# Kernel optimization log

Hardware: AMD Instinct MI355X
Metric: run time of the kernel (lower is better)

## Reference

```python
import jax, jax.numpy as jnp
import numpy as np

DIM = 512
DIM_HEAD = 32
HEADS = DIM // DIM_HEAD
WS = 8  # window (partition) size
INNER = (DIM * 4 * 2 // 3 // 32) * 32  # gated-MLP inner dim = 2720
EPS = 1e-6
LS_INIT = 1e-5


def _ln(x, g, b):
    mu = jnp.mean(x, axis=-1, keepdims=True)
    var = jnp.var(x, axis=-1, keepdims=True)
    return (x - mu) * jax.lax.rsqrt(var + EPS) * g + b


def setup_inputs() -> dict:
    key = jax.random.key(0)
    ks = jax.random.split(key, 8)
    B, H, W = 8, 96, 96
    s = lambda d: 1.0 / np.sqrt(d)
    return {
        "x": jax.random.normal(ks[0], (B, H, W, DIM), jnp.float32),
        "norm1_g": jnp.ones((DIM,), jnp.float32),
        "norm1_b": jnp.zeros((DIM,), jnp.float32),
        "qkv_w": jax.random.normal(ks[1], (DIM, 3 * DIM), jnp.float32) * s(DIM),
        "qkv_b": jnp.zeros((3 * DIM,), jnp.float32),
        "proj_w": jax.random.normal(ks[2], (DIM, DIM), jnp.float32) * s(DIM),
        "proj_b": jnp.zeros((DIM,), jnp.float32),
        "ls1": jnp.full((DIM,), LS_INIT, jnp.float32),
        "norm2_g": jnp.ones((DIM,), jnp.float32),
        "norm2_b": jnp.zeros((DIM,), jnp.float32),
        "glu_w": jax.random.normal(ks[3], (DIM, 2 * INNER), jnp.float32) * s(DIM),
        "glu_b": jnp.zeros((2 * INNER,), jnp.float32),
        "fc2_w": jax.random.normal(ks[4], (INNER, DIM), jnp.float32) * s(INNER),
        "fc2_b": jnp.zeros((DIM,), jnp.float32),
        "ls2": jnp.full((DIM,), LS_INIT, jnp.float32),
    }


def reference(x, norm1_g, norm1_b, qkv_w, qkv_b, proj_w, proj_b, ls1,
              norm2_g, norm2_b, glu_w, glu_b, fc2_w, fc2_b, ls2):
    B, H, W, C = x.shape
    nH, nW = H // WS, W // WS
    T = WS * WS  # tokens per window

    # ---- window attention branch ----
    y = _ln(x, norm1_g, norm1_b)
    # window_partition: (B,H,W,C) -> (B*nH*nW, T, C)
    y = y.reshape(B, nH, WS, nW, WS, C).transpose(0, 1, 3, 2, 4, 5)
    y = y.reshape(-1, T, C)
    qkv = y @ qkv_w + qkv_b                      # (M, T, 3C)
    qkv = qkv.reshape(-1, T, 3, HEADS, DIM_HEAD)
    q, k, v = qkv[:, :, 0], qkv[:, :, 1], qkv[:, :, 2]   # (M, T, h, d)
    scale = DIM_HEAD ** -0.5
    attn = jnp.einsum('mqhd,mkhd->mhqk', q, k) * scale
    attn = jax.nn.softmax(attn, axis=-1)
    o = jnp.einsum('mhqk,mkhd->mqhd', attn, v).reshape(-1, T, C)
    o = o @ proj_w + proj_b
    # window_reverse: (M, T, C) -> (B, H, W, C)
    o = o.reshape(B, nH, nW, WS, WS, C).transpose(0, 1, 3, 2, 4, 5)
    o = o.reshape(B, H, W, C)
    x = x + ls1 * o

    # ---- gated MLP branch (GLU with SiLU) ----
    y = _ln(x, norm2_g, norm2_b)
    h = y @ glu_w + glu_b
    h, gate = jnp.split(h, 2, axis=-1)
    h = h * jax.nn.silu(gate)
    h = h @ fc2_w + fc2_b
    x = x + ls2 * h
    return x
```

## Files before the change

### kernel.cpp

```cpp
#include <hip/hip_runtime.h>
#include <hip/hip_bf16.h>
#include <stdint.h>
#include <math.h>

#define DIM 512
#define INNER 1344
#define INNERP 1408

typedef __attribute__((ext_vector_type(8))) short vbf8;
typedef __attribute__((ext_vector_type(4))) float vf4;
typedef __attribute__((ext_vector_type(4))) int v4i;
typedef __attribute__((ext_vector_type(8))) int v8i;

typedef __attribute__((address_space(1))) void as1void;
typedef __attribute__((address_space(3))) void as3void;

union frag8 {
  v8i w;
  v4i h[2];
};

__device__ __forceinline__ uint32_t quant4(float v) {
  uint32_t s = (__float_as_uint(v) >> 31) << 3;
  float a = fabsf(v);
  uint32_t m = (a > 0.25f) + (a > 0.75f) + (a > 1.25f) + (a > 1.75f) +
               (a > 2.5f) + (a > 3.5f) + (a > 5.0f);
  return s | m;
}
__device__ __forceinline__ uint32_t pack8fp4(const float* r) {
  uint32_t u = 0;
#pragma unroll
  for (int j = 0; j < 8; ++j) u |= quant4(r[j]) << (4 * j);
  return u;
}

#define MFMA4(a, b, c, sb) \
  __builtin_amdgcn_mfma_scale_f32_16x16x128_f8f6f4((a), (b), (c), 4, 4, 0, 127, 0, (sb))

__global__ void k_transpose4(const float* __restrict__ Wsrc, uint8_t* __restrict__ WT,
                             uint8_t* __restrict__ Wsc, int K, int N, int ldB, int ldS,
                             int nsplit) {
  __shared__ float tile[32][33];
  const int tx = threadIdx.x, ty = threadIdx.y;
  const int n0 = blockIdx.x * 32, k0 = blockIdx.y * 32;
#pragma unroll
  for (int i = 0; i < 32; i += 8) {
    int k = k0 + ty + i, n = n0 + tx;
    if (k < K && n < N) tile[ty + i][tx] = Wsrc[(size_t)k * N + n];
  }
  __syncthreads();
  if (tx < 16) {
#pragma unroll
    for (int i = 0; i < 32; i += 8) {
      int n = n0 + ty + i;
      if (n >= N) continue;
      float v0 = tile[2 * tx][ty + i], v1 = tile[2 * tx + 1][ty + i];
      float m = fmaxf(fabsf(v0), fabsf(v1));
      m = fmaxf(m, __shfl_xor(m, 1));
      m = fmaxf(m, __shfl_xor(m, 2));
      m = fmaxf(m, __shfl_xor(m, 4));
      m = fmaxf(m, __shfl_xor(m, 8));
      uint8_t sbyte;
      float s;
      if (m < 1e-20f) {
        sbyte = 0;
        s = 0.0f;
      } else {
        int e = (int)ceilf(log2f(m * 0.166666672f));
        e = e < -126 ? -126 : (e > 126 ? 126 : e);
        sbyte = (uint8_t)(e + 127);
        s = exp2f((float)(-e));
      }
      int np = n + (n >= nsplit ? 64 : 0);
      WT[(size_t)np * ldB + (k0 >> 1) + tx] =
          (uint8_t)(quant4(v0 * s) | (quant4(v1 * s) << 4));
      if (tx == 0) Wsc[(size_t)np * ldS + (k0 >> 5)] = sbyte;
    }
  }
}

__global__ void k_padbias(const float* __restrict__ b, float* __restrict__ o) {
  int c = blockIdx.x * 256 + threadIdx.x;
  if (c < INNER) o[c] = b[c];
  else if (c >= INNERP && c < INNERP + INNER) o[c] = b[c - 64];
  else if (c < 2816) o[c] = 0.0f;
}

template <bool PART, bool BF16IN>
__global__ __launch_bounds__(256) void k_ln(const void* __restrict__ xin,
                                            const float* __restrict__ gw,
                                            const float* __restrict__ bw,
                                            uint8_t* __restrict__ y) {
  const int wave = threadIdx.x >> 6, lane = threadIdx.x & 63;
  const int tok = blockIdx.x * 4 + wave;
  float vals[8];
  if (BF16IN) {
    const __hip_bfloat16* xr = (const __hip_bfloat16*)xin + (size_t)tok * DIM + lane * 8;
    union {
      vbf8 v;
      ushort e[8];
    } u;
    u.v = *(const vbf8*)xr;
#pragma unroll
    for (int j = 0; j < 8; ++j) vals[j] = __uint_as_float((unsigned)u.e[j] << 16);
  } else {
    const float* xr = (const float*)xin + (size_t)tok * DIM + lane * 8;
    const float4 v0 = *(const float4*)xr;
    const float4 v1 = *(const float4*)(xr + 4);
    vals[0] = v0.x; vals[1] = v0.y; vals[2] = v0.z; vals[3] = v0.w;
    vals[4] = v1.x; vals[5] = v1.y; vals[6] = v1.z; vals[7] = v1.w;
  }
  float s = 0.f, ss = 0.f;
#pragma unroll
  for (int j = 0; j < 8; ++j) {
    s += vals[j];
    ss += vals[j] * vals[j];
  }
#pragma unroll
  for (int off = 32; off > 0; off >>= 1) {
    s += __shfl_xor(s, off);
    ss += __shfl_xor(ss, off);
  }
  const float mu = s * (1.0f / DIM);
  const float rs = rsqrtf(ss * (1.0f / DIM) - mu * mu + 1e-6f);
  size_t orow;
  if (PART) {
    int b = tok / 9216, rem = tok % 9216;
    int h = rem / 96, w = rem % 96;
    orow = (size_t)(((b * 12 + (h >> 3)) * 12 + (w >> 3)) * 64 + (h & 7) * 8 + (w & 7));
  } else {
    orow = (size_t)tok;
  }
  const float4 g0 = *(const float4*)(gw + lane * 8);
  const float4 g1 = *(const float4*)(gw + lane * 8 + 4);
  const float4 b0 = *(const float4*)(bw + lane * 8);
  const float4 b1 = *(const float4*)(bw + lane * 8 + 4);
  const float gg[8] = {g0.x, g0.y, g0.z, g0.w, g1.x, g1.y, g1.z, g1.w};
  const float bb[8] = {b0.x, b0.y, b0.z, b0.w, b1.x, b1.y, b1.z, b1.w};
  float r[8];
#pragma unroll
  for (int j = 0; j < 8; ++j) r[j] = (vals[j] - mu) * rs * gg[j] + bb[j];
  *(uint32_t*)(y + orow * 256 + lane * 4) = pack8fp4(r);
}

template <int ROWS>
__device__ __forceinline__ void stage4(const uint8_t* __restrict__ gsrc, int RB, char* lds,
                                       int wave, int lane) {
  constexpr int RPW = ROWS / 4;
  const int r0 = wave * RPW;
  const int srw = lane >> 2, sbk = lane & 3;
  const uint8_t* src = gsrc + (size_t)(r0 + srw) * RB + ((sbk ^ (srw & 3)) << 4);
  char* dst = lds + r0 * 64;
#pragma unroll
  for (int c = 0; c < RPW; c += 16)
    __builtin_amdgcn_global_load_lds((const as1void*)(src + (size_t)c * RB),
                                     (as3void*)(dst + c * 64), 16, 0, 0);
}

template <int MODE, int NT>
__global__ __launch_bounds__(256, 3) void k_gemm4(const uint8_t* __restrict__ A4,
                                                  const uint8_t* __restrict__ B4,
                                                  const uint8_t* __restrict__ Bsc,
                                                  const float* __restrict__ bias,
                                                  void* __restrict__ outp,
                                                  const void* __restrict__ resid,
                                                  const float* __restrict__ lsv, const int K,
                                                  const int ldOut) {
  __shared__ alignas(16) char As[128 * 64];
  __shared__ alignas(16) char Bs[128 * 64];
  const int nwg = gridDim.x;
  int bid = blockIdx.x;
  bid = (bid & 7) * (nwg >> 3) + (bid >> 3);
  const int bm = bid / NT, bn = bid % NT;
  const int tid = threadIdx.x, wave = tid >> 6, lane = tid & 63;
  const int wr = wave >> 1, wc = wave & 1;
  const int cl = lane & 15, g = lane >> 4;
  const int RB = K >> 1, KB = K >> 5, nkt = K >> 7;

  const uint8_t* Ab = A4 + (size_t)bm * 128 * RB;
  const uint8_t* Bb = B4 + (size_t)bn * 128 * RB;

  int aoff[4], boff[4];
  const uint8_t* bscp[4];
#pragma unroll
  for (int i = 0; i < 4; ++i) {
    int ra = wr * 64 + cl + i * 16;
    int rb = wc * 64 + cl + i * 16;
    aoff[i] = ra * 64 + ((g ^ (ra & 3)) << 4);
    boff[i] = rb * 64 + ((g ^ (rb & 3)) << 4);
    bscp[i] = Bsc + (size_t)(bn * 128 + rb) * KB + g;
  }

  frag8 afr[4], bfr[4];
#pragma unroll
  for (int i = 0; i < 4; ++i) {
    afr[i].w = (v8i){0, 0, 0, 0, 0, 0, 0, 0};
    bfr[i].w = (v8i){0, 0, 0, 0, 0, 0, 0, 0};
  }
  vf4 acc[4][4] = {};

  for (int t = 0; t < nkt; ++t) {
    __syncthreads();
    stage4<128>(Ab + t * 64, RB, As, wave, lane);
    stage4<128>(Bb + t * 64, RB, Bs, wave, lane);
    __syncthreads();
    int sb[4];
#pragma unroll
    for (int i = 0; i < 4; ++i) sb[i] = (int)bscp[i][t * 4];
#pragma unroll
    for (int i = 0; i < 4; ++i) {
      afr[i].h[0] = *(const v4i*)(As + aoff[i]);
      bfr[i].h[0] = *(const v4i*)(Bs + boff[i]);
    }
#pragma unroll
    for (int mi = 0; mi < 4; ++mi)
#pragma unroll
      for (int ni = 0; ni < 4; ++ni)
        acc[mi][ni] = MFMA4(afr[mi].w, bfr[ni].w, acc[mi][ni], sb[ni]);
  }

  const int rl = g << 2;
  const int rbase = bm * 128 + wr * 64;
  const int cbase = bn * 128 + wc * 64;
#pragma unroll
  for (int mi = 0; mi < 4; ++mi) {
#pragma unroll
    for (int j = 0; j < 4; ++j) {
      const int r = rbase + mi * 16 + rl + j;
      size_t orow;
      if (MODE == 1) {
        int m = r >> 6, t = r & 63;
        int b = m / 144, mm = m % 144;
        int wh = mm / 12, ww = mm % 12;
        int h = wh * 8 + (t >> 3), w = ww * 8 + (t & 7);
        orow = (size_t)((b * 96 + h) * 96 + w);
      } else {
        orow = (size_t)r;
      }
#pragma unroll
      for (int ni = 0; ni < 4; ++ni) {
        const int c = cbase + ni * 16 + cl;
        const float v = acc[mi][ni][j] + bias[c];
        if (MODE == 0) {
          ((__hip_bfloat16*)outp)[(size_t)r * ldOut + c] = __float2bfloat16(v);
        } else if (MODE == 1) {
          const float* rx = (const float*)resid;
          ((__hip_bfloat16*)outp)[orow * DIM + c] =
              __float2bfloat16(rx[orow * DIM + c] + lsv[c] * v);
        } else {
          const __hip_bfloat16* rx = (const __hip_bfloat16*)resid;
          ((float*)outp)[(size_t)r * DIM + c] =
              __bfloat162float(rx[(size_t)r * DIM + c]) + lsv[c] * v;
        }
      }
    }
  }
}

__global__ __launch_bounds__(256, 3) void k_gemm_glu4(const uint8_t* __restrict__ A4,
                                                      const uint8_t* __restrict__ B4,
                                                      const uint8_t* __restrict__ Bsc,
                                                      const float* __restrict__ bias,
                                                      uint8_t* __restrict__ hout) {
  __shared__ alignas(16) char As[128 * 64];
  __shared__ alignas(16) char B0s[64 * 64];
  __shared__ alignas(16) char B1s[64 * 64];
  __shared__ float pane[4][64][17];
  const int K = DIM, RB = 256, KB = 16;
  const int nwg = gridDim.x;
  int bid = blockIdx.x;
  bid = (bid & 7) * (nwg >> 3) + (bid >> 3);
  const int bm = bid / 22, bn = bid % 22;
  const int tid = threadIdx.x, wave = tid >> 6, lane = tid & 63;
  const int wr = wave >> 1, wc = wave & 1;
  const int cl = lane & 15, g = lane >> 4;

  const uint8_t* Ab = A4 + (size_t)bm * 128 * RB;
  const uint8_t* Bb0 = B4 + (size_t)(bn * 64) * RB;
  const uint8_t* Bb1 = B4 + (size_t)(INNERP + bn * 64) * RB;

  int aoff[4], boff[2];
  const uint8_t* b0scp[2];
  const uint8_t* b1scp[2];
#pragma unroll
  for (int i = 0; i < 4; ++i) {
    int ra = wr * 64 + cl + i * 16;
    aoff[i] = ra * 64 + ((g ^ (ra & 3)) << 4);
  }
#pragma unroll
  for (int i = 0; i < 2; ++i) {
    int rb = wc * 32 + cl + i * 16;
    boff[i] = rb * 64 + ((g ^ (rb & 3)) << 4);
    b0scp[i] = Bsc + (size_t)(bn * 64 + rb) * KB + g;
    b1scp[i] = Bsc + (size_t)(INNERP + bn * 64 + rb) * KB + g;
  }

  frag8 afr[4], b0f[2], b1f[2];
#pragma unroll
  for (int i = 0; i < 4; ++i) afr[i].w = (v8i){0, 0, 0, 0, 0, 0, 0, 0};
#pragma unroll
  for (int i = 0; i < 2; ++i) {
    b0f[i].w = (v8i){0, 0, 0, 0, 0, 0, 0, 0};
    b1f[i].w = (v8i){0, 0, 0, 0, 0, 0, 0, 0};
  }
  vf4 a0[4][2] = {}, a1[4][2] = {};

#pragma unroll
  for (int t = 0; t < 4; ++t) {
    __syncthreads();
    stage4<128>(Ab + t * 64, RB, As, wave, lane);
    stage4<64>(Bb0 + t * 64, RB, B0s, wave, lane);
    stage4<64>(Bb1 + t * 64, RB, B1s, wave, lane);
    __syncthreads();
    int sb0[2], sb1[2];
#pragma unroll
    for (int i = 0; i < 2; ++i) {
      sb0[i] = (int)b0scp[i][t * 4];
      sb1[i] = (int)b1scp[i][t * 4];
    }
#pragma unroll
    for (int i = 0; i < 4; ++i) afr[i].h[0] = *(const v4i*)(As + aoff[i]);
#pragma unroll
    for (int i = 0; i < 2; ++i) {
      b0f[i].h[0] = *(const v4i*)(B0s + boff[i]);
      b1f[i].h[0] = *(const v4i*)(B1s + boff[i]);
    }
#pragma unroll
    for (int mi = 0; mi < 4; ++mi)
#pragma unroll
      for (int ni = 0; ni < 2; ++ni) {
        a0[mi][ni] = MFMA4(afr[mi].w, b0f[ni].w, a0[mi][ni], sb0[ni]);
        a1[mi][ni] = MFMA4(afr[mi].w, b1f[ni].w, a1[mi][ni], sb1[ni]);
      }
  }

  const int rbase = bm * 128 + wr * 64;
  const int cbase = bn * 64 + wc * 32;
#pragma unroll
  for (int ni = 0; ni < 2; ++ni) {
#pragma unroll
    for (int mi = 0; mi < 4; ++mi)
#pragma unroll
      for (int j = 0; j < 4; ++j) {
        const int c = cbase + ni * 16 + cl;
        const float a = a0[mi][ni][j] + bias[c];
        const float gv = a1[mi][ni][j] + bias[INNERP + c];
        const float sg = 1.0f / (1.0f + __expf(-gv));
        pane[wave][mi * 16 + g * 4 + j][cl] = a * gv * sg;
      }
    asm volatile("s_waitcnt lgkmcnt(0)" ::: "memory");
    __builtin_amdgcn_sched_barrier(0);
    {
      const float* pr = &pane[wave][lane][0];
      float v0[8], v1[8];
#pragma unroll
      for (int b = 0; b < 8; ++b) {
        v0[b] = pr[b];
        v1[b] = pr[8 + b];
      }
      uint8_t* hp = hout + (size_t)(rbase + lane) * 704 + ((cbase + ni * 16) >> 1);
      *(uint32_t*)hp = pack8fp4(v0);
      *(uint32_t*)(hp + 4) = pack8fp4(v1);
    }
    asm volatile("s_waitcnt lgkmcnt(0)" ::: "memory");
    __builtin_amdgcn_sched_barrier(0);
  }
}

__global__ __launch_bounds__(256, 2) void k_attn_mfma(const __hip_bfloat16* __restrict__ qkv,
                                                      uint8_t* __restrict__ o) {
  __shared__ __hip_bfloat16 sm[4][6912];
  const int wave = threadIdx.x >> 6, lane = threadIdx.x & 63;
  const int task = blockIdx.x * 4 + wave;
  const int w = task >> 4, hd = task & 15;
  const int g = lane >> 4, c = lane & 15;
  __hip_bfloat16* smp = sm[wave];
  __hip_bfloat16* smv = smp + 4608;

  const __hip_bfloat16* base = qkv + (size_t)w * 64 * 1536 + hd * 32;

  vbf8 qf[4], kf[4];
#pragma unroll
  for (int i = 0; i < 4; ++i) {
    const __hip_bfloat16* qrow = base + (size_t)(i * 16 + c) * 1536 + g * 8;
    qf[i] = *(const vbf8*)qrow;
    kf[i] = *(const vbf8*)(qrow + 512);
  }

  {
    const __hip_bfloat16* vrow = base + (size_t)lane * 1536 + 1024;
    union {
      vbf8 v;
      ushort e[8];
    } uv[4];
#pragma unroll
    for (int i = 0; i < 4; ++i) uv[i].v = *(const vbf8*)(vrow + i * 8);
#pragma unroll
    for (int d = 0; d < 32; ++d)
      ((ushort*)smv)[d * 72 + lane] = uv[d >> 3].e[d & 7];
  }

  vf4 st[4][4];
#pragma unroll
  for (int iq = 0; iq < 4; ++iq)
#pragma unroll
    for (int it = 0; it < 4; ++it) {
      vf4 z = {};
      st[iq][it] = __builtin_amdgcn_mfma_f32_16x16x32_bf16(qf[iq], kf[it], z, 0, 0, 0);
    }

  float inv[4][4];
#pragma unroll
  for (int iq = 0; iq < 4; ++iq) {
#pragma unroll
    for (int j = 0; j < 4; ++j) {
      float m = fmaxf(fmaxf(st[iq][0][j], st[iq][1][j]), fmaxf(st[iq][2][j], st[iq][3][j]));
      m = fmaxf(m, __shfl_xor(m, 1));
      m = fmaxf(m, __shfl_xor(m, 2));
      m = fmaxf(m, __shfl_xor(m, 4));
      m = fmaxf(m, __shfl_xor(m, 8));
      float s = 0.f;
#pragma unroll
      for (int it = 0; it < 4; ++it) {
        const float e = __expf((st[iq][it][j] - m) * 0.17677669529663687f);
        st[iq][it][j] = e;
        s += e;
      }
      s += __shfl_xor(s, 1);
      s += __shfl_xor(s, 2);
      s += __shfl_xor(s, 4);
      s += __shfl_xor(s, 8);
      inv[iq][j] = 1.0f / s;
    }
  }

#pragma unroll
  for (int iq = 0; iq < 4; ++iq)
#pragma unroll
    for (int j = 0; j < 4; ++j) {
      const int q = iq * 16 + g * 4 + j;
#pragma unroll
      for (int it = 0; it < 4; ++it)
        smp[q * 72 + it * 16 + c] = __float2bfloat16(st[iq][it][j]);
    }

  vf4 ot[4][2] = {};
#pragma unroll
  for (int ks = 0; ks < 2; ++ks) {
    vbf8 pf[4], vfr[2];
#pragma unroll
    for (int iq = 0; iq < 4; ++iq)
      pf[iq] = *(const vbf8*)(smp + (iq * 16 + c) * 72 + ks * 32 + g * 8);
#pragma unroll
    for (int dt = 0; dt < 2; ++dt)
      vfr[dt] = *(const vbf8*)(smv + (dt * 16 + c) * 72 + ks * 32 + g * 8);
#pragma unroll
    for (int iq = 0; iq < 4; ++iq)
#pragma unroll
      for (int dt = 0; dt < 2; ++dt)
        ot[iq][dt] = __builtin_amdgcn_mfma_f32_16x16x32_bf16(pf[iq], vfr[dt], ot[iq][dt], 0, 0, 0);
  }

#pragma unroll
  for (int iq = 0; iq < 4; ++iq)
#pragma unroll
    for (int dt = 0; dt < 2; ++dt)
#pragma unroll
      for (int j = 0; j < 4; ++j) {
        const int q = iq * 16 + g * 4 + j;
        smp[q * 72 + dt * 16 + c] = __float2bfloat16(ot[iq][dt][j] * inv[iq][j]);
      }
  uint8_t* ob = o + (size_t)w * 64 * 256 + hd * 16;
#pragma unroll
  for (int i = 0; i < 4; ++i) {
    const int idx = i * 64 + lane;
    const int row = idx >> 2, chunk = idx & 3;
    union {
      vbf8 v;
      ushort e[8];
    } u;
    u.v = *(const vbf8*)(smp + row * 72 + chunk * 8);
    float f[8];
#pragma unroll
    for (int j = 0; j < 8; ++j) f[j] = __uint_as_float((unsigned)u.e[j] << 16);
    *(uint32_t*)(ob + (size_t)row * 256 + chunk * 4) = pack8fp4(f);
  }
}

extern "C" void kernel_launch(void* const* d_in, const int* in_sizes, int n_in, void* d_out,
                              int out_size, void* d_ws, size_t ws_size, hipStream_t stream) {
  const float* x = (const float*)d_in[0];
  const float* n1g = (const float*)d_in[1];
  const float* n1b = (const float*)d_in[2];
  const float* qkv_w = (const float*)d_in[3];
  const float* qkv_b = (const float*)d_in[4];
  const float* proj_w = (const float*)d_in[5];
  const float* proj_b = (const float*)d_in[6];
  const float* ls1 = (const float*)d_in[7];
  const float* n2g = (const float*)d_in[8];
  const float* n2b = (const float*)d_in[9];
  const float* glu_w = (const float*)d_in[10];
  const float* glu_b = (const float*)d_in[11];
  const float* fc2_w = (const float*)d_in[12];
  const float* fc2_b = (const float*)d_in[13];
  const float* ls2 = (const float*)d_in[14];

  if (ws_size < 248000000u) return;

  char* ws = (char*)d_ws;
  uint8_t* wTq4 = (uint8_t*)(ws + 0);
  uint8_t* wTp4 = (uint8_t*)(ws + 393216);
  uint8_t* wTg4 = (uint8_t*)(ws + 524288);
  uint8_t* wTf4 = (uint8_t*)(ws + 1245184);
  uint8_t* sq = (uint8_t*)(ws + 1605632);
  uint8_t* sp = (uint8_t*)(ws + 1630208);
  uint8_t* sg = (uint8_t*)(ws + 1638400);
  uint8_t* sf = (uint8_t*)(ws + 1683456);
  float* gbias = (float*)(ws + 1705984);
  uint8_t* act4 = (uint8_t*)(ws + 2097152);
  char* big = ws + 20971520;
  __hip_bfloat16* qkvbuf = (__hip_bfloat16*)big;
  uint8_t* h4 = (uint8_t*)big;
  __hip_bfloat16* x1b = (__hip_bfloat16*)(big + 69206016);

  hipMemsetAsync(wTg4, 0, 720896, stream);
  hipMemsetAsync(wTf4, 0, 360448, stream);
  hipMemsetAsync(sg, 0, 45056, stream);
  hipMemsetAsync(sf, 0, 22528, stream);

  dim3 tb(32, 8);
  k_transpose4<<<dim3(48, 16), tb, 0, stream>>>(qkv_w, wTq4, sq, 512, 1536, 256, 16, 1 << 30);
  k_transpose4<<<dim3(16, 16), tb, 0, stream>>>(proj_w, wTp4, sp, 512, 512, 256, 16, 1 << 30);
  k_transpose4<<<dim3(84, 16), tb, 0, stream>>>(glu_w, wTg4, sg, 512, 2688, 256, 16, INNER);
  k_transpose4<<<dim3(16, 42), tb, 0, stream>>>(fc2_w, wTf4, sf, 1344, 512, 704, 44, 1 << 30);
  k_padbias<<<11, 256, 0, stream>>>(glu_b, gbias);

  k_ln<true, false><<<18432, 256, 0, stream>>>(x, n1g, n1b, act4);
  k_gemm4<0, 12><<<6912, 256, 0, stream>>>(act4, wTq4, sq, qkv_b, qkvbuf, nullptr, nullptr, 512, 1536);
  k_attn_mfma<<<4608, 256, 0, stream>>>(qkvbuf, act4);
  k_gemm4<1, 4><<<2304, 256, 0, stream>>>(act4, wTp4, sp, proj_b, (void*)x1b, x, ls1, 512, 512);
  k_ln<false, true><<<18432, 256, 0, stream>>>(x1b, n2g, n2b, act4);
  k_gemm_glu4<<<12672, 256, 0, stream>>>(act4, wTg4, sg, gbias, h4);
  k_gemm4<2, 4><<<2304, 256, 0, stream>>>(h4, wTf4, sf, fc2_b, d_out, x1b, ls2, 1408, 512);
}
```

Before: 571.5 us.

## Switch activations from FP4 to FP8 in mixed-precision scaled MFMA GEMMs

Activations (LN outputs, attention output, GLU hidden) are now stored as FP8 e4m3 via hardware pack-convert instructions instead of a software FP4 quantizer, while weights stay FP4. The GEMMs use mixed-format scaled MFMA (A fp8, B fp4) with a new 128-byte-row LDS staging and swizzle for A, and the GLU epilogue writes bytes directly instead of going through an LDS pane. The aim is cheaper quantization and better accuracy, at the cost of twice the activation bytes, more LDS per block, and lower occupancy (launch bounds reduced to 2).

Result: no change. 570.1 us (-0.2%).

```diff
diff --git a/kernel.cpp b/kernel.cpp
--- a/kernel.cpp
+++ b/kernel.cpp
@@ -19,6 +19,12 @@
   v8i w;
   v4i h[2];
 };
+
+__device__ __forceinline__ unsigned pk4fp8(float a, float b, float c, float d) {
+  int v = __builtin_amdgcn_cvt_pk_fp8_f32(a, b, 0, false);
+  v = __builtin_amdgcn_cvt_pk_fp8_f32(c, d, v, true);
+  return (unsigned)v;
+}
 
 __device__ __forceinline__ uint32_t quant4(float v) {
   uint32_t s = (__float_as_uint(v) >> 31) << 3;
@@ -27,15 +33,9 @@
                (a > 2.5f) + (a > 3.5f) + (a > 5.0f);
   return s | m;
 }
-__device__ __forceinline__ uint32_t pack8fp4(const float* r) {
-  uint32_t u = 0;
-#pragma unroll
-  for (int j = 0; j < 8; ++j) u |= quant4(r[j]) << (4 * j);
-  return u;
-}
-
-#define MFMA4(a, b, c, sb) \
-  __builtin_amdgcn_mfma_scale_f32_16x16x128_f8f6f4((a), (b), (c), 4, 4, 0, 127, 0, (sb))
+
+#define MFMA_M(a, b, c, sb) \
+  __builtin_amdgcn_mfma_scale_f32_16x16x128_f8f6f4((a), (b), (c), 0, 4, 0, 127, 0, (sb))
 
 __global__ void k_transpose4(const float* __restrict__ Wsrc, uint8_t* __restrict__ WT,
                              uint8_t* __restrict__ Wsc, int K, int N, int ldB, int ldS,
@@ -140,33 +140,62 @@
   float r[8];
 #pragma unroll
   for (int j = 0; j < 8; ++j) r[j] = (vals[j] - mu) * rs * gg[j] + bb[j];
-  *(uint32_t*)(y + orow * 256 + lane * 4) = pack8fp4(r);
+  uint2 po;
+  po.x = pk4fp8(r[0], r[1], r[2], r[3]);
+  po.y = pk4fp8(r[4], r[5], r[6], r[7]);
+  *(uint2*)(y + orow * DIM + lane * 8) = po;
 }
 
 template <int ROWS>
-__device__ __forceinline__ void stage4(const uint8_t* __restrict__ gsrc, int RB, char* lds,
+__device__ __forceinline__ void stage8(const uint8_t* __restrict__ g, int ldKb, char* lds,
+                                       int wave, int lane) {
+  constexpr int RPW = ROWS / 4;
+  const int r0 = wave * RPW;
+  const int ro = lane >> 3;
+  const int pb = lane & 7;
+  const uint8_t* src = g + (size_t)(r0 + ro) * (size_t)ldKb + ((pb ^ ro) << 4);
+  char* dst = lds + r0 * 128;
+#pragma unroll
+  for (int c = 0; c < RPW; c += 8)
+    __builtin_amdgcn_global_load_lds((const as1void*)(src + (size_t)c * (size_t)ldKb),
+                                     (as3void*)(dst + c * 128), 16, 0, 0);
+}
+__device__ __forceinline__ v8i fragA8(const char* base, int row, int g) {
+  const int ro = row & 7;
+  const v4i lo = *(const v4i*)(base + row * 128 + (((2 * g) ^ ro) << 4));
+  const v4i hi = *(const v4i*)(base + row * 128 + (((2 * g + 1) ^ ro) << 4));
+  return __builtin_shufflevector(lo, hi, 0, 1, 2, 3, 4, 5, 6, 7);
+}
+
+template <int ROWS>
+__device__ __forceinline__ void stage4(const uint8_t* __restrict__ g, int ldKb, char* lds,
                                        int wave, int lane) {
   constexpr int RPW = ROWS / 4;
   const int r0 = wave * RPW;
   const int srw = lane >> 2, sbk = lane & 3;
-  const uint8_t* src = gsrc + (size_t)(r0 + srw) * RB + ((sbk ^ (srw & 3)) << 4);
+  const int fsw = (srw + (srw >> 2)) & 3;
+  const uint8_t* src = g + (size_t)(r0 + srw) * (size_t)ldKb + ((sbk ^ fsw) << 4);
   char* dst = lds + r0 * 64;
 #pragma unroll
   for (int c = 0; c < RPW; c += 16)
-    __builtin_amdgcn_global_load_lds((const as1void*)(src + (size_t)c * RB),
+    __builtin_amdgcn_global_load_lds((const as1void*)(src + (size_t)c * (size_t)ldKb),
                                      (as3void*)(dst + c * 64), 16, 0, 0);
 }
+__device__ __forceinline__ v4i fragB4(const char* base, int row, int g) {
+  const int f = (row + (row >> 2)) & 3;
+  return *(const v4i*)(base + row * 64 + ((g ^ f) << 4));
+}
 
 template <int MODE, int NT>
-__global__ __launch_bounds__(256, 3) void k_gemm4(const uint8_t* __restrict__ A4,
-                                                  const uint8_t* __restrict__ B4,
-                                                  const uint8_t* __restrict__ Bsc,
-                                                  const float* __restrict__ bias,
-                                                  void* __restrict__ outp,
-                                                  const void* __restrict__ resid,
-                                                  const float* __restrict__ lsv, const int K,
-                                                  const int ldOut) {
-  __shared__ alignas(16) char As[128 * 64];
+__global__ __launch_bounds__(256, 2) void k_gemm_m(const uint8_t* __restrict__ A8,
+                                                   const uint8_t* __restrict__ B4,
+                                                   const uint8_t* __restrict__ Bsc,
+                                                   const float* __restrict__ bias,
+                                                   void* __restrict__ outp,
+                                                   const void* __restrict__ resid,
+                                                   const float* __restrict__ lsv, const int K,
+                                                   const int ldOut) {
+  __shared__ alignas(16) char As[128 * 128];
   __shared__ alignas(16) char Bs[128 * 64];
   const int nwg = gridDim.x;
   int bid = blockIdx.x;
@@ -175,48 +204,40 @@
   const int tid = threadIdx.x, wave = tid >> 6, lane = tid & 63;
   const int wr = wave >> 1, wc = wave & 1;
   const int cl = lane & 15, g = lane >> 4;
-  const int RB = K >> 1, KB = K >> 5, nkt = K >> 7;
-
-  const uint8_t* Ab = A4 + (size_t)bm * 128 * RB;
-  const uint8_t* Bb = B4 + (size_t)bn * 128 * RB;
-
-  int aoff[4], boff[4];
+  const int KB = K >> 5, nkt = K >> 7;
+
+  const uint8_t* Ab = A8 + (size_t)bm * 128 * K;
+  const uint8_t* Bb = B4 + (size_t)bn * 128 * (K >> 1);
+
   const uint8_t* bscp[4];
 #pragma unroll
-  for (int i = 0; i < 4; ++i) {
-    int ra = wr * 64 + cl + i * 16;
-    int rb = wc * 64 + cl + i * 16;
-    aoff[i] = ra * 64 + ((g ^ (ra & 3)) << 4);
-    boff[i] = rb * 64 + ((g ^ (rb & 3)) << 4);
-    bscp[i] = Bsc + (size_t)(bn * 128 + rb) * KB + g;
-  }
-
-  frag8 afr[4], bfr[4];
-#pragma unroll
-  for (int i = 0; i < 4; ++i) {
-    afr[i].w = (v8i){0, 0, 0, 0, 0, 0, 0, 0};
-    bfr[i].w = (v8i){0, 0, 0, 0, 0, 0, 0, 0};
-  }
+  for (int i = 0; i < 4; ++i)
+    bscp[i] = Bsc + (size_t)(bn * 128 + wc * 64 + cl + i * 16) * KB + g;
+
+  frag8 bfr[4];
+#pragma unroll
+  for (int i = 0; i < 4; ++i) bfr[i].w = (v8i){0, 0, 0, 0, 0, 0, 0, 0};
   vf4 acc[4][4] = {};
 
   for (int t = 0; t < nkt; ++t) {
     __syncthreads();
-    stage4<128>(Ab + t * 64, RB, As, wave, lane);
-    stage4<128>(Bb + t * 64, RB, Bs, wave, lane);
+    stage8<128>(Ab + t * 128, K, As, wave, lane);
+    stage4<128>(Bb + t * 64, K >> 1, Bs, wave, lane);
     __syncthreads();
     int sb[4];
 #pragma unroll
     for (int i = 0; i < 4; ++i) sb[i] = (int)bscp[i][t * 4];
+    v8i af[4];
 #pragma unroll
     for (int i = 0; i < 4; ++i) {
-      afr[i].h[0] = *(const v4i*)(As + aoff[i]);
-      bfr[i].h[0] = *(const v4i*)(Bs + boff[i]);
+      af[i] = fragA8(As, wr * 64 + cl + i * 16, g);
+      bfr[i].h[0] = fragB4(Bs, wc * 64 + cl + i * 16, g);
     }
 #pragma unroll
     for (int mi = 0; mi < 4; ++mi)
 #pragma unroll
       for (int ni = 0; ni < 4; ++ni)
-        acc[mi][ni] = MFMA4(afr[mi].w, bfr[ni].w, acc[mi][ni], sb[ni]);
+        acc[mi][ni] = MFMA_M(af[mi], bfr[ni].w, acc[mi][ni], sb[ni]);
   }
 
   const int rl = g << 2;
@@ -257,16 +278,15 @@
   }
 }
 
-__global__ __launch_bounds__(256, 3) void k_gemm_glu4(const uint8_t* __restrict__ A4,
-                                                      const uint8_t* __restrict__ B4,
-                                                      const uint8_t* __restrict__ Bsc,
-                                                      const float* __restrict__ bias,
-                                                      uint8_t* __restrict__ hout) {
-  __shared__ alignas(16) char As[128 * 64];
+__global__ __launch_bounds__(256, 2) void k_gemm_glu_m(const uint8_t* __restrict__ A8,
+                                                       const uint8_t* __restrict__ B4,
+                                                       const uint8_t* __restrict__ Bsc,
+                                                       const float* __restrict__ bias,
+                                                       uint8_t* __restrict__ hout) {
+  __shared__ alignas(16) char As[128 * 128];
   __shared__ alignas(16) char B0s[64 * 64];
   __shared__ alignas(16) char B1s[64 * 64];
-  __shared__ float pane[4][64][17];
-  const int K = DIM, RB = 256, KB = 16;
+  const int K = DIM, KB = 16;
   const int nwg = gridDim.x;
   int bid = blockIdx.x;
   bid = (bid & 7) * (nwg >> 3) + (bid >> 3);
@@ -275,29 +295,20 @@
   const int wr = wave >> 1, wc = wave & 1;
   const int cl = lane & 15, g = lane >> 4;
 
-  const uint8_t* Ab = A4 + (size_t)bm * 128 * RB;
-  const uint8_t* Bb0 = B4 + (size_t)(bn * 64) * RB;
-  const uint8_t* Bb1 = B4 + (size_t)(INNERP + bn * 64) * RB;
-
-  int aoff[4], boff[2];
+  const uint8_t* Ab = A8 + (size_t)bm * 128 * K;
+  const uint8_t* Bb0 = B4 + (size_t)(bn * 64) * 256;
+  const uint8_t* Bb1 = B4 + (size_t)(INNERP + bn * 64) * 256;
+
   const uint8_t* b0scp[2];
   const uint8_t* b1scp[2];
 #pragma unroll
-  for (int i = 0; i < 4; ++i) {
-    int ra = wr * 64 + cl + i * 16;
-    aoff[i] = ra * 64 + ((g ^ (ra & 3)) << 4);
-  }
-#pragma unroll
   for (int i = 0; i < 2; ++i) {
     int rb = wc * 32 + cl + i * 16;
-    boff[i] = rb * 64 + ((g ^ (rb & 3)) << 4);
     b0scp[i] = Bsc + (size_t)(bn * 64 + rb) * KB + g;
     b1scp[i] = Bsc + (size_t)(INNERP + bn * 64 + rb) * KB + g;
   }
 
-  frag8 afr[4], b0f[2], b1f[2];
-#pragma unroll
-  for (int i = 0; i < 4; ++i) afr[i].w = (v8i){0, 0, 0, 0, 0, 0, 0, 0};
+  frag8 b0f[2], b1f[2];
 #pragma unroll
   for (int i = 0; i < 2; ++i) {
     b0f[i].w = (v8i){0, 0, 0, 0, 0, 0, 0, 0};
@@ -308,9 +319,9 @@
 #pragma unroll
   for (int t = 0; t < 4; ++t) {
     __syncthreads();
-    stage4<128>(Ab + t * 64, RB, As, wave, lane);
-    stage4<64>(Bb0 + t * 64, RB, B0s, wave, lane);
-    stage4<64>(Bb1 + t * 64, RB, B1s, wave, lane);
+    stage8<128>(Ab + t * 128, K, As, wave, lane);
+    stage4<64>(Bb0 + t * 64, 256, B0s, wave, lane);
+    stage4<64>(Bb1 + t * 64, 256, B1s, wave, lane);
     __syncthreads();
     int sb0[2], sb1[2];
 #pragma unroll
@@ -318,53 +329,42 @@
       sb0[i] = (int)b0scp[i][t * 4];
       sb1[i] = (int)b1scp[i][t * 4];
     }
-#pragma unroll
-    for (int i = 0; i < 4; ++i) afr[i].h[0] = *(const v4i*)(As + aoff[i]);
+    v8i af[4];
+#pragma unroll
+    for (int i = 0; i < 4; ++i) af[i] = fragA8(As, wr * 64 + cl + i * 16, g);
 #pragma unroll
     for (int i = 0; i < 2; ++i) {
-      b0f[i].h[0] = *(const v4i*)(B0s + boff[i]);
-      b1f[i].h[0] = *(const v4i*)(B1s + boff[i]);
+      b0f[i].h[0] = fragB4(B0s, wc * 32 + cl + i * 16, g);
+      b1f[i].h[0] = fragB4(B1s, wc * 32 + cl + i * 16, g);
     }
 #pragma unroll
     for (int mi = 0; mi < 4; ++mi)
 #pragma unroll
       for (int ni = 0; ni < 2; ++ni) {
-        a0[mi][ni] = MFMA4(afr[mi].w, b0f[ni].w, a0[mi][ni], sb0[ni]);
-        a1[mi][ni] = MFMA4(afr[mi].w, b1f[ni].w, a1[mi][ni], sb1[ni]);
-      }
-  }
-
+        a0[mi][ni] = MFMA_M(af[mi], b0f[ni].w, a0[mi][ni], sb0[ni]);
+        a1[mi][ni] = MFMA_M(af[mi], b1f[ni].w, a1[mi][ni], sb1[ni]);
+      }
+  }
+
+  const int rl = g << 2;
   const int rbase = bm * 128 + wr * 64;
   const int cbase = bn * 64 + wc * 32;
 #pragma unroll
-  for (int ni = 0; ni < 2; ++ni) {
-#pragma unroll
-    for (int mi = 0; mi < 4; ++mi)
-#pragma unroll
-      for (int j = 0; j < 4; ++j) {
+  for (int mi = 0; mi < 4; ++mi)
+#pragma unroll
+    for (int j = 0; j < 4; ++j) {
+      const int r = rbase + mi * 16 + rl + j;
+#pragma unroll
+      for (int ni = 0; ni < 2; ++ni) {
         const int c = cbase + ni * 16 + cl;
         const float a = a0[mi][ni][j] + bias[c];
         const float gv = a1[mi][ni][j] + bias[INNERP + c];
         const float sg = 1.0f / (1.0f + __expf(-gv));
-        pane[wave][mi * 16 + g * 4 + j][cl] = a * gv * sg;
-      }
-    asm volatile("s_waitcnt lgkmcnt(0)" ::: "memory");
-    __builtin_amdgcn_sched_barrier(0);
-    {
-      const float* pr = &pane[wave][lane][0];
-      float v0[8], v1[8];
-#pragma unroll
-      for (int b = 0; b < 8; ++b) {
-        v0[b] = pr[b];
-        v1[b] = pr[8 + b];
-      }
-      uint8_t* hp = hout + (size_t)(rbase + lane) * 704 + ((cbase + ni * 16) >> 1);
-      *(uint32_t*)hp = pack8fp4(v0);
-      *(uint32_t*)(hp + 4) = pack8fp4(v1);
-    }
-    asm volatile("s_waitcnt lgkmcnt(0)" ::: "memory");
-    __builtin_amdgcn_sched_barrier(0);
-  }
+        const float hv = a * gv * sg;
+        hout[(size_t)r * INNERP + c] =
+            (uint8_t)(__builtin_amdgcn_cvt_pk_fp8_f32(hv, hv, 0, false) & 0xff);
+      }
+    }
 }
 
 __global__ __launch_bounds__(256, 2) void k_attn_mfma(const __hip_bfloat16* __restrict__ qkv,
@@ -470,7 +470,7 @@
         const int q = iq * 16 + g * 4 + j;
         smp[q * 72 + dt * 16 + c] = __float2bfloat16(ot[iq][dt][j] * inv[iq][j]);
       }
-  uint8_t* ob = o + (size_t)w * 64 * 256 + hd * 16;
+  uint8_t* ob = o + (size_t)w * 64 * 512 + hd * 32;
 #pragma unroll
   for (int i = 0; i < 4; ++i) {
     const int idx = i * 64 + lane;
@@ -483,7 +483,10 @@
     float f[8];
 #pragma unroll
     for (int j = 0; j < 8; ++j) f[j] = __uint_as_float((unsigned)u.e[j] << 16);
-    *(uint32_t*)(ob + (size_t)row * 256 + chunk * 4) = pack8fp4(f);
+    uint2 pv;
+    pv.x = pk4fp8(f[0], f[1], f[2], f[3]);
+    pv.y = pk4fp8(f[4], f[5], f[6], f[7]);
+    *(uint2*)(ob + (size_t)row * 512 + chunk * 8) = pv;
   }
 }
 
@@ -505,7 +508,7 @@
   const float* fc2_b = (const float*)d_in[13];
   const float* ls2 = (const float*)d_in[14];
 
-  if (ws_size < 248000000u) return;
+  if (ws_size < 268000000u) return;
 
   char* ws = (char*)d_ws;
   uint8_t* wTq4 = (uint8_t*)(ws + 0);
@@ -517,11 +520,11 @@
   uint8_t* sg = (uint8_t*)(ws + 1638400);
   uint8_t* sf = (uint8_t*)(ws + 1683456);
   float* gbias = (float*)(ws + 1705984);
-  uint8_t* act4 = (uint8_t*)(ws + 2097152);
-  char* big = ws + 20971520;
+  uint8_t* act8 = (uint8_t*)(ws + 2097152);
+  char* big = ws + 39845888;
   __hip_bfloat16* qkvbuf = (__hip_bfloat16*)big;
-  uint8_t* h4 = (uint8_t*)big;
-  __hip_bfloat16* x1b = (__hip_bfloat16*)(big + 69206016);
+  uint8_t* h8 = (uint8_t*)big;
+  __hip_bfloat16* x1b = (__hip_bfloat16*)(big + 109051904);
 
   hipMemsetAsync(wTg4, 0, 720896, stream);
   hipMemsetAsync(wTf4, 0, 360448, stream);
@@ -535,11 +538,11 @@
   k_transpose4<<<dim3(16, 42), tb, 0, stream>>>(fc2_w, wTf4, sf, 1344, 512, 704, 44, 1 << 30);
   k_padbias<<<11, 256, 0, stream>>>(glu_b, gbias);
 
-  k_ln<true, false><<<18432, 256, 0, stream>>>(x, n1g, n1b, act4);
-  k_gemm4<0, 12><<<6912, 256, 0, stream>>>(act4, wTq4, sq, qkv_b, qkvbuf, nullptr, nullptr, 512, 1536);
-  k_attn_mfma<<<4608, 256, 0, stream>>>(qkvbuf, act4);
-  k_gemm4<1, 4><<<2304, 256, 0, stream>>>(act4, wTp4, sp, proj_b, (void*)x1b, x, ls1, 512, 512);
-  k_ln<false, true><<<18432, 256, 0, stream>>>(x1b, n2g, n2b, act4);
-  k_gemm_glu4<<<12672, 256, 0, stream>>>(act4, wTg4, sg, gbias, h4);
-  k_gemm4<2, 4><<<2304, 256, 0, stream>>>(h4, wTf4, sf, fc2_b, d_out, x1b, ls2, 1408, 512);
-}
+  k_ln<true, false><<<18432, 256, 0, stream>>>(x, n1g, n1b, act8);
+  k_gemm_m<0, 12><<<6912, 256, 0, stream>>>(act8, wTq4, sq, qkv_b, qkvbuf, nullptr, nullptr, 512, 1536);
+  k_attn_mfma<<<4608, 256, 0, stream>>>(qkvbuf, act8);
+  k_gemm_m<1, 4><<<2304, 256, 0, stream>>>(act8, wTp4, sp, proj_b, (void*)x1b, x, ls1, 512, 512);
+  k_ln<false, true><<<18432, 256, 0, stream>>>(x1b, n2g, n2b, act8);
+  k_gemm_glu_m<<<12672, 256, 0, stream>>>(act8, wTg4, sg, gbias, h8);
+  k_gemm_m<2, 4><<<2304, 256, 0, stream>>>(h8, wTf4, sf, fc2_b, d_out, x1b, ls2, INNERP, 512);
+}
```
